# Kernel tuning notes

Measured on AMD Instinct MI355X. Metric: run time of the kernel, lower is better.

Reference implementation:

```python
import jax, jax.numpy as jnp
import numpy as np

H_OUT, W_OUT = 48, 320


def setup_inputs() -> dict:
    key = jax.random.key(0)
    k1, k2, k3 = jax.random.split(key, 3)
    x = jax.random.normal(k1, (8, 64, 200, 320), dtype=jnp.float32)
    bboxes = jax.random.randint(k2, (256, 4), 0, 320, dtype=jnp.int32)
    box_img = jax.random.randint(k3, (256,), 0, 8, dtype=jnp.int32)
    return {"x": x, "bboxes": bboxes, "box_img": box_img}


def reference(x, bboxes, box_img):
    # x: [B, C, H, W]; bboxes: [N, 4] int (x0, y0, x1, y1); box_img: [N] image index
    B, C, H, W = x.shape
    x0 = jnp.clip(bboxes[:, 0], 0, W - 1)
    y0 = jnp.clip(bboxes[:, 1], 0, H - 1)
    x1 = jnp.clip(bboxes[:, 2], 0, W - 1)
    y1 = jnp.clip(bboxes[:, 3], 0, H - 1)
    x1 = jnp.maximum(x1, x0)
    y1 = jnp.maximum(y1, y0)
    # inclusive crop: height/width of each crop
    h = y1 - y0 + 1  # [N]
    w = x1 - x0 + 1  # [N]
    # F.interpolate default mode='nearest': src = floor(dst * in/out)
    i = jnp.arange(H_OUT, dtype=jnp.int32)
    j = jnp.arange(W_OUT, dtype=jnp.int32)
    rows = y0[:, None] + (i[None, :] * h[:, None]) // H_OUT  # [N, H_OUT]
    cols = x0[:, None] + (j[None, :] * w[:, None]) // W_OUT  # [N, W_OUT]
    # single fused gather: advanced indices broadcast to [N, H_OUT, W_OUT],
    # with the ':' channel slice moved to the last axis -> [N, H_OUT, W_OUT, C]
    g = x[box_img[:, None, None], :, rows[:, :, None], cols[:, None, :]]
    return jnp.transpose(g, (0, 3, 1, 2))  # [N, C, H_OUT, W_OUT]
```

## Files before the change

kernel.cpp:

```cpp
#include <hip/hip_runtime.h>

#define C_CH   64
#define H_IN   200
#define W_IN   320
#define H_OUT  48
#define W_OUT  320
#define N_BOX  256

__global__ __launch_bounds__(320, 8) void roi_crop_kernel(
    const float* __restrict__ x,
    const int*   __restrict__ bboxes,
    const int*   __restrict__ box_img,
    float*       __restrict__ out)
{
    const int box = blockIdx.x;
    const int c   = blockIdx.y;
    const int t   = threadIdx.x;

    int x0 = bboxes[box * 4 + 0];
    int y0 = bboxes[box * 4 + 1];
    int x1 = bboxes[box * 4 + 2];
    int y1 = bboxes[box * 4 + 3];

    x0 = min(max(x0, 0), W_IN - 1);
    y0 = min(max(y0, 0), H_IN - 1);
    x1 = min(max(x1, 0), W_IN - 1);
    y1 = min(max(y1, 0), H_IN - 1);
    x1 = max(x1, x0);
    y1 = max(y1, y0);

    const int h   = y1 - y0 + 1;
    const int w   = x1 - x0 + 1;
    const int img = box_img[box];

    const float* __restrict__ plane_in =
        x + ((size_t)img * C_CH + c) * (H_IN * W_IN);
    float* __restrict__ plane_out =
        out + ((size_t)box * C_CH + c) * (H_OUT * W_OUT);

    const int col = x0 + (t * w) / W_OUT;
    const float* __restrict__ src = plane_in + col;
    float*       __restrict__ dst = plane_out + t;

    #pragma unroll 8
    for (int i = 0; i < H_OUT; ++i) {
        const int r = y0 + (i * h) / H_OUT;
        const float val = src[r * W_IN];
        __builtin_nontemporal_store(val, dst + i * W_OUT);
    }
}

extern "C" void kernel_launch(void* const* d_in, const int* in_sizes, int n_in,
                              void* d_out, int out_size, void* d_ws, size_t ws_size,
                              hipStream_t stream) {
    const float* x       = (const float*)d_in[0];
    const int*   bboxes  = (const int*)d_in[1];
    const int*   box_img = (const int*)d_in[2];
    float*       out     = (float*)d_out;

    dim3 grid(N_BOX, C_CH);
    dim3 block(320);
    roi_crop_kernel<<<grid, block, 0, stream>>>(x, bboxes, box_img, out);
}
```

Measured before the change: 1.126 ms.

## Stage source rows into LDS via async global_load_lds with double buffering

Instead of each thread gathering one scattered float per output row, whole source rows for chunks of eight output rows are copied into LDS with 16-byte async global-to-LDS loads, double-buffered across chunks. The column gather then reads from LDS before the nontemporal global store. The aim is to replace uncoalesced, duplicated global reads with full-width coalesced row loads and to overlap them with the stores. The cost is extra block barriers, hand-written vmcnt waits whose counts must match the issued loads, dropped occupancy hints, and reading full 320-wide rows even when the box is narrow.

```diff
diff --git a/kernel.cpp b/kernel.cpp
--- a/kernel.cpp
+++ b/kernel.cpp
@@ -1,4 +1,5 @@
 #include <hip/hip_runtime.h>
+#include <stdint.h>
 
 #define C_CH   64
 #define H_IN   200
@@ -6,26 +7,34 @@
 #define H_OUT  48
 #define W_OUT  320
 #define N_BOX  256
+#define CHUNK  8
+#define NCHUNK (H_OUT / CHUNK)
 
-__global__ __launch_bounds__(320, 8) void roi_crop_kernel(
+
+typedef __attribute__((address_space(3))) void       lds_vp;
+typedef __attribute__((address_space(1))) const void gbl_vp;
+
+__device__ __forceinline__ void glds16(const float* g, float* l) {
+    __builtin_amdgcn_global_load_lds((gbl_vp*)g, (lds_vp*)l, 16, 0, 0);
+}
+
+__global__ __launch_bounds__(320) void roi_crop_kernel(
     const float* __restrict__ x,
     const int*   __restrict__ bboxes,
     const int*   __restrict__ box_img,
     float*       __restrict__ out)
 {
+    __shared__ __align__(16) float tile[2][CHUNK * W_OUT];
+
     const int box = blockIdx.x;
     const int c   = blockIdx.y;
     const int t   = threadIdx.x;
 
-    int x0 = bboxes[box * 4 + 0];
-    int y0 = bboxes[box * 4 + 1];
-    int x1 = bboxes[box * 4 + 2];
-    int y1 = bboxes[box * 4 + 3];
-
-    x0 = min(max(x0, 0), W_IN - 1);
-    y0 = min(max(y0, 0), H_IN - 1);
-    x1 = min(max(x1, 0), W_IN - 1);
-    y1 = min(max(y1, 0), H_IN - 1);
+    const int4 bb = *(const int4*)(bboxes + box * 4);
+    int x0 = min(max(bb.x, 0), W_IN - 1);
+    int y0 = min(max(bb.y, 0), H_IN - 1);
+    int x1 = min(max(bb.z, 0), W_IN - 1);
+    int y1 = min(max(bb.w, 0), H_IN - 1);
     x1 = max(x1, x0);
     y1 = max(y1, y0);
 
@@ -38,15 +47,51 @@
     float* __restrict__ plane_out =
         out + ((size_t)box * C_CH + c) * (H_OUT * W_OUT);
 
-    const int col = x0 + (t * w) / W_OUT;
-    const float* __restrict__ src = plane_in + col;
-    float*       __restrict__ dst = plane_out + t;
+    const int wave  = t >> 6;
+    const int lane  = t & 63;
+    const int pbase = wave * 2048 + lane * 16;
+    const int col   = x0 + (t * w) / W_OUT;
 
-    #pragma unroll 8
-    for (int i = 0; i < H_OUT; ++i) {
-        const int r = y0 + (i * h) / H_OUT;
-        const float val = src[r * W_IN];
-        __builtin_nontemporal_store(val, dst + i * W_OUT);
+    auto stage = [&](int k, int nb) {
+        #pragma unroll
+        for (int q = 0; q < 2; ++q) {
+            const int p   = pbase + (q << 10);
+            const int rl  = p / 1280;
+            const int off = p - rl * 1280;
+            const int r   = y0 + ((k * CHUNK + rl) * h) / H_OUT;
+            glds16(plane_in + r * W_IN + (off >> 2),
+                   &tile[nb][wave * 512 + (q << 8)]);
+        }
+    };
+
+    stage(0, 0);
+    __builtin_amdgcn_sched_barrier(0);
+
+    #pragma unroll
+    for (int k = 0; k < NCHUNK; ++k) {
+        const int nb = k & 1;
+        if (k + 1 < NCHUNK) stage(k + 1, nb ^ 1);
+        __builtin_amdgcn_sched_barrier(0);
+        if (k == 0)
+            asm volatile("s_waitcnt vmcnt(2)" ::: "memory");
+        else if (k + 1 < NCHUNK)
+            asm volatile("s_waitcnt vmcnt(10)" ::: "memory");
+        else
+            asm volatile("s_waitcnt vmcnt(8)" ::: "memory");
+        __builtin_amdgcn_sched_barrier(0);
+        __builtin_amdgcn_s_barrier();
+        __builtin_amdgcn_sched_barrier(0);
+
+        float* op = plane_out + (size_t)(k * CHUNK) * W_OUT + t;
+        #pragma unroll
+        for (int il = 0; il < CHUNK; ++il) {
+            const float v = tile[nb][il * W_OUT + col];
+            __builtin_nontemporal_store(v, op + il * W_OUT);
+        }
+
+        __builtin_amdgcn_sched_barrier(0);
+        __builtin_amdgcn_s_barrier();
+        __builtin_amdgcn_sched_barrier(0);
     }
 }
 
```

Result: no change. 1.113 ms (-1.2%).

## Stage unique source rows in LDS via direct global-to-LDS loads, emit float4 stores

Applied to the files above, without the earlier changes.

Each block now loads only the distinct source rows needed for its crop (up to 48) as 16-byte chunks straight into LDS with global_load_lds. Output is then produced from LDS with float4-vectorized stores instead of scalar nontemporal stores. This removes redundant global reads when several output rows or columns map to the same source and widens the store path. In exchange it adds a barrier and 61KB of LDS per block, which lowers occupancy, and it drops the nontemporal hint.

```diff
diff --git a/kernel.cpp b/kernel.cpp
--- a/kernel.cpp
+++ b/kernel.cpp
@@ -7,25 +7,32 @@
 #define W_OUT  320
 #define N_BOX  256
 
-__global__ __launch_bounds__(320, 8) void roi_crop_kernel(
+typedef float float4v __attribute__((ext_vector_type(4), aligned(16)));
+
+typedef __attribute__((address_space(3))) void       lds_vp;
+typedef __attribute__((address_space(1))) const void gbl_vp;
+
+__device__ __forceinline__ void glds16(const float* g, float* l) {
+    __builtin_amdgcn_global_load_lds((gbl_vp*)g, (lds_vp*)l, 16, 0, 0);
+}
+
+__global__ __launch_bounds__(320) void roi_crop_kernel(
     const float* __restrict__ x,
     const int*   __restrict__ bboxes,
     const int*   __restrict__ box_img,
     float*       __restrict__ out)
 {
+    __shared__ __align__(16) float tile[H_OUT * 80 * 4];
+
     const int box = blockIdx.x;
     const int c   = blockIdx.y;
     const int t   = threadIdx.x;
 
-    int x0 = bboxes[box * 4 + 0];
-    int y0 = bboxes[box * 4 + 1];
-    int x1 = bboxes[box * 4 + 2];
-    int y1 = bboxes[box * 4 + 3];
-
-    x0 = min(max(x0, 0), W_IN - 1);
-    y0 = min(max(y0, 0), H_IN - 1);
-    x1 = min(max(x1, 0), W_IN - 1);
-    y1 = min(max(y1, 0), H_IN - 1);
+    const int4 bb = *(const int4*)(bboxes + box * 4);
+    int x0 = min(max(bb.x, 0), W_IN - 1);
+    int y0 = min(max(bb.y, 0), H_IN - 1);
+    int x1 = min(max(bb.z, 0), W_IN - 1);
+    int y1 = min(max(bb.w, 0), H_IN - 1);
     x1 = max(x1, x0);
     y1 = max(y1, y0);
 
@@ -38,15 +45,36 @@
     float* __restrict__ plane_out =
         out + ((size_t)box * C_CH + c) * (H_OUT * W_OUT);
 
-    const int col = x0 + (t * w) / W_OUT;
-    const float* __restrict__ src = plane_in + col;
-    float*       __restrict__ dst = plane_out + t;
+    const int x0f4 = x0 >> 2;
+    const int K4   = (x1 >> 2) - x0f4 + 1;
+    const int x0f  = x0f4 << 2;
+    const int nur  = (h < H_OUT) ? h : H_OUT;
+    const bool small_h = (h <= H_OUT);
 
-    #pragma unroll 8
-    for (int i = 0; i < H_OUT; ++i) {
-        const int r = y0 + (i * h) / H_OUT;
-        const float val = src[r * W_IN];
-        __builtin_nontemporal_store(val, dst + i * W_OUT);
+    for (int s = 0; s < nur; ++s) {
+        const int rs = small_h ? (y0 + s) : (y0 + (s * h) / H_OUT);
+        if (t < K4)
+            glds16(plane_in + (size_t)rs * W_IN + x0f + (t << 2),
+                   &tile[(s * K4 + t) << 2]);
+    }
+    __syncthreads();
+
+    const int ldrow = K4 << 2;
+    float4v* __restrict__ out4 = (float4v*)plane_out;
+    #pragma unroll
+    for (int k = 0; k < 12; ++k) {
+        const int p = t + k * 320;
+        const int i = p / 80;
+        const int u = p - i * 80;
+        const int s = small_h ? (i * h) / H_OUT : i;
+        const int base = s * ldrow - x0f;
+        float4v v;
+        #pragma unroll
+        for (int e = 0; e < 4; ++e) {
+            const int ce = x0 + ((4 * u + e) * w) / W_OUT;
+            v[e] = tile[base + ce];
+        }
+        out4[p] = v;
     }
 }
 
```

Measured after the change: 1.114 ms. No clear change (-1.1%).
